# Kernel tuning notes

Measured on AMD Instinct MI355X. Metric: run time of the kernel, lower is better.

Reference implementation:

```python
import jax, jax.numpy as jnp
import numpy as np

N_NODES = 100000
N_EDGES = 1600000
N_ETYPES = 3
IN_FEATS = 128
HEADS = 4
OUT_FEATS = 16
EDGE_FEATS = 64
NEG_SLOPE = 0.2


def setup_inputs() -> dict:
    key = jax.random.key(0)
    ks = jax.random.split(key, 10)
    return {
        "x": jax.random.normal(ks[0], (N_NODES, IN_FEATS), jnp.float32),
        "W": jax.random.normal(ks[1], (IN_FEATS, HEADS * OUT_FEATS), jnp.float32) * 0.05,
        "W_e": jax.random.normal(ks[2], (EDGE_FEATS, HEADS * EDGE_FEATS), jnp.float32) * 0.05,
        "attn_l": jax.random.normal(ks[3], (HEADS, OUT_FEATS), jnp.float32) * 0.1,
        "attn_r": jax.random.normal(ks[4], (HEADS, OUT_FEATS), jnp.float32) * 0.1,
        "attn_e": jax.random.normal(ks[5], (HEADS, EDGE_FEATS), jnp.float32) * 0.1,
        "edge_emb": jax.random.normal(ks[6], (N_ETYPES, EDGE_FEATS), jnp.float32),
        "src": jax.random.randint(ks[7], (N_EDGES,), 0, N_NODES, jnp.int32),
        "dst": jax.random.randint(ks[8], (N_EDGES,), 0, N_NODES, jnp.int32),
        "etype": jax.random.randint(ks[9], (N_EDGES,), 0, N_ETYPES, jnp.int32),
    }


def reference(x, W, W_e, attn_l, attn_r, attn_e, edge_emb, src, dst, etype):
    N = x.shape[0]
    H, D = attn_l.shape
    # node projection: [N, H, D]
    feat = (x @ W).reshape(N, H, D)
    # per-node attention halves: [N, H]
    el = jnp.einsum("nhd,hd->nh", feat, attn_l)
    er = jnp.einsum("nhd,hd->nh", feat, attn_r)
    # per-etype edge term: [T, H]
    e_feat = (edge_emb @ W_e).reshape(edge_emb.shape[0], H, -1)
    ee = jnp.einsum("the,he->th", e_feat, attn_e)
    # per-edge pre-softmax score: [E, H]
    s = el[src] + er[dst] + ee[etype]
    s = jnp.where(s > 0, s, NEG_SLOPE * s)  # leaky_relu
    # edge softmax over incoming edges of each dst node (homogeneous graph)
    m = jax.ops.segment_max(s, dst, num_segments=N)
    e = jnp.exp(s - m[dst])
    z = jax.ops.segment_sum(e, dst, num_segments=N)
    a = e / z[dst]  # [E, H]
    # u_mul_e + sum aggregation: [N, H, D]
    msg = feat[src] * a[:, :, None]
    rst = jax.ops.segment_sum(msg, dst, num_segments=N)
    return rst, a
```

## Files before the change

kernel.cpp:

```cpp
#include <hip/hip_runtime.h>
#include <hip/hip_bf16.h>

#define N_NODES   100000
#define N_EDGES   1600000
#define N_ETYPES  3
#define IN_FEATS  128
#define HEADS     4
#define OUT_FEATS 16
#define EDGE_FEATS 64
#define HD        64
#define NEG_SLOPE 0.2f
#define MAXD_LDS  128

#define NBUCK     800
#define NPB       125
#define PBLK      400
#define EPB       4000
#define BCAP      2560


typedef short s16x8 __attribute__((ext_vector_type(8)));
typedef float f32x4 __attribute__((ext_vector_type(4)));

__device__ __forceinline__ short f2bs(float f) {
    __hip_bfloat16 h = __float2bfloat16(f);
    return *reinterpret_cast<short*>(&h);
}

__global__ __launch_bounds__(256) void wt_prep_kernel(
    const float* __restrict__ W, short* __restrict__ WTb)
{
    const int t = blockIdx.x * 256 + threadIdx.x;
    const int k = t >> 6, n = t & 63;
    WTb[n * IN_FEATS + k] = f2bs(W[t]);
}

#define XS_STRIDE 136
__global__ __launch_bounds__(256) void feat_el_er_kernel(
    const float* __restrict__ x,
    const short* __restrict__ WTb,
    const float* __restrict__ attn_l,
    const float* __restrict__ attn_r,
    __hip_bfloat16* __restrict__ featb,
    float* __restrict__ el,
    float* __restrict__ eriz)
{
    __shared__ short Xs[16 * XS_STRIDE];
    __shared__ short Ws[64 * XS_STRIDE];

    const int t = threadIdx.x;
    const int row0 = blockIdx.x * 16;
    {
        const int r = t >> 4, k0 = (t & 15) * 8;
        const float4* xg = (const float4*)(x + (size_t)(row0 + r) * IN_FEATS + k0);
        const float4 v0 = xg[0], v1 = xg[1];
        s16x8 p;
        p[0] = f2bs(v0.x); p[1] = f2bs(v0.y); p[2] = f2bs(v0.z); p[3] = f2bs(v0.w);
        p[4] = f2bs(v1.x); p[5] = f2bs(v1.y); p[6] = f2bs(v1.z); p[7] = f2bs(v1.w);
        *(s16x8*)&Xs[r * XS_STRIDE + k0] = p;
    }
    {
#pragma unroll
        for (int j = 0; j < 4; ++j) {
            const int u = t + 256 * j;
            const int r = u >> 4, c = (u & 15) * 8;
            *(s16x8*)&Ws[r * XS_STRIDE + c] = *(const s16x8*)(WTb + r * IN_FEATS + c);
        }
    }
    __syncthreads();

    const int w    = t >> 6;
    const int lane = t & 63;
    const int m    = lane & 15;
    const int q    = lane >> 4;

    f32x4 acc = {0.f, 0.f, 0.f, 0.f};
#pragma unroll
    for (int kb = 0; kb < 4; ++kb) {
        const s16x8 af = *(const s16x8*)&Xs[m * XS_STRIDE + kb * 32 + q * 8];
        const s16x8 bf = *(const s16x8*)&Ws[(w * 16 + m) * XS_STRIDE + kb * 32 + q * 8];
        acc = __builtin_amdgcn_mfma_f32_16x16x32_bf16(af, bf, acc, 0, 0, 0);
    }

    const float al = attn_l[w * OUT_FEATS + m];
    const float ar = attn_r[w * OUT_FEATS + m];
#pragma unroll
    for (int r = 0; r < 4; ++r) {
        const int row = row0 + q * 4 + r;
        featb[(size_t)row * HD + w * 16 + m] = __float2bfloat16(acc[r]);
        float cl = acc[r] * al;
        float cr = acc[r] * ar;
#pragma unroll
        for (int msk = 1; msk < 16; msk <<= 1) {
            cl += __shfl_xor(cl, msk, 64);
            cr += __shfl_xor(cr, msk, 64);
        }
        if (m == 0) {
            el[row * HEADS + w] = cl;
            eriz[(size_t)row * 8 + w] = cr;
        }
    }
}

__global__ __launch_bounds__(64) void ee_kernel(
    const float* __restrict__ edge_emb,
    const float* __restrict__ W_e,
    const float* __restrict__ attn_e,
    float* __restrict__ ee)
{
    const int b  = blockIdx.x;
    const int ty = b >> 2;
    const int h  = b & 3;
    const int e  = threadIdx.x;

    float ef = 0.f;
#pragma unroll
    for (int k = 0; k < EDGE_FEATS; ++k)
        ef += edge_emb[ty * EDGE_FEATS + k] *
              W_e[k * (HEADS * EDGE_FEATS) + h * EDGE_FEATS + e];
    float v = ef * attn_e[h * EDGE_FEATS + e];
#pragma unroll
    for (int m = 1; m < 64; m <<= 1) v += __shfl_xor(v, m, 64);
    if (e == 0) ee[ty * HEADS + h] = v;
}

__global__ __launch_bounds__(256) void bucket_hist_kernel(
    const int* __restrict__ dst, int* __restrict__ bhist)
{
    __shared__ int h[NBUCK];
    const int t = threadIdx.x, b = blockIdx.x;
    for (int j = t; j < NBUCK; j += 256) h[j] = 0;
    __syncthreads();
    const int e0 = b * EPB;
    for (int i = t; i < EPB; i += 256)
        atomicAdd(&h[dst[e0 + i] / NPB], 1);
    __syncthreads();
    for (int j = t; j < NBUCK; j += 256) bhist[b * NBUCK + j] = h[j];
}

__global__ __launch_bounds__(256) void bucket_scan1_kernel(
    int* __restrict__ bhist, int* __restrict__ btot)
{
    __shared__ int sh[PBLK];
    const int t = threadIdx.x, j = blockIdx.x;
    const int j0 = t, j1 = t + 256;
    int o0 = 0, o1 = 0;
    if (j0 < PBLK) { o0 = bhist[j0 * NBUCK + j]; sh[j0] = o0; }
    if (j1 < PBLK) { o1 = bhist[j1 * NBUCK + j]; sh[j1] = o1; }
    __syncthreads();
    for (int off = 1; off < PBLK; off <<= 1) {
        int v0 = (j0 >= off && j0 < PBLK) ? sh[j0 - off] : 0;
        int v1 = (j1 >= off && j1 < PBLK) ? sh[j1 - off] : 0;
        __syncthreads();
        if (j0 < PBLK) sh[j0] += v0;
        if (j1 < PBLK) sh[j1] += v1;
        __syncthreads();
    }
    if (j0 < PBLK) bhist[j0 * NBUCK + j] = sh[j0] - o0;
    if (j1 < PBLK) bhist[j1 * NBUCK + j] = sh[j1] - o1;
    if (t == 255) btot[j] = sh[PBLK - 1];
}

__global__ __launch_bounds__(1024) void bucket_scan2_kernel(
    const int* __restrict__ btot, int* __restrict__ bbase)
{
    __shared__ int sh[NBUCK];
    const int t = threadIdx.x;
    int o = 0;
    if (t < NBUCK) { o = btot[t]; sh[t] = o; }
    __syncthreads();
    for (int off = 1; off < NBUCK; off <<= 1) {
        int v = (t >= off && t < NBUCK) ? sh[t - off] : 0;
        __syncthreads();
        if (t < NBUCK) sh[t] += v;
        __syncthreads();
    }
    if (t < NBUCK) bbase[t] = sh[t] - o;
    if (t == NBUCK - 1) bbase[NBUCK] = sh[t];
}

__global__ __launch_bounds__(256) void bucket_scatter_kernel(
    const int* __restrict__ src, const int* __restrict__ dst,
    const int* __restrict__ etype,
    const int* __restrict__ bhist, const int* __restrict__ bbase,
    int* __restrict__ sc_bucket)
{
    __shared__ int cnt[NBUCK];
    const int t = threadIdx.x, b = blockIdx.x;
    for (int j = t; j < NBUCK; j += 256)
        cnt[j] = bbase[j] + bhist[b * NBUCK + j];
    __syncthreads();
    const int e0 = b * EPB;
    for (int i = t; i < EPB; i += 256) {
        const int e  = e0 + i;
        const int dn = dst[e];
        const int bu = dn / NPB;
        const int ld = dn - bu * NPB;
        const int slot = atomicAdd(&cnt[bu], 1);
        sc_bucket[slot] = src[e] | (etype[e] << 17) | (ld << 19);
    }
}

__global__ __launch_bounds__(256) void bucket_csr_kernel(
    const int* __restrict__ sc_bucket, const int* __restrict__ bbase,
    int* __restrict__ ptr, int* __restrict__ sc_csr)
{
    __shared__ int sbuf[BCAP];
    __shared__ int sdeg[128];
    __shared__ int scur[128];
    const int t = threadIdx.x, b = blockIdx.x;
    const int lo = bbase[b];
    const int count = bbase[b + 1] - lo;
    const bool staged = (count <= BCAP);

    if (t < 128) sdeg[t] = 0;
    __syncthreads();
    if (staged) {
        for (int i = t; i < count; i += 256) {
            const int v = sc_bucket[lo + i];
            sbuf[i] = v;
            atomicAdd(&sdeg[(v >> 19) & 0x7F], 1);
        }
    } else {
        for (int i = t; i < count; i += 256)
            atomicAdd(&sdeg[(sc_bucket[lo + i] >> 19) & 0x7F], 1);
    }
    __syncthreads();
    const int orig = (t < 128) ? sdeg[t] : 0;
    for (int off = 1; off < 128; off <<= 1) {
        const int v = (t < 128 && t >= off) ? sdeg[t - off] : 0;
        __syncthreads();
        if (t < 128) sdeg[t] += v;
        __syncthreads();
    }
    if (t < 128) {
        const int excl = sdeg[t] - orig;
        if (t < NPB) ptr[b * NPB + t] = lo + excl;
        scur[t] = lo + excl;
    }
    if (b == 0 && t == 0) ptr[N_NODES] = N_EDGES;
    __syncthreads();
    if (staged) {
        for (int i = t; i < count; i += 256) {
            const int v = sbuf[i];
            const int ld = (v >> 19) & 0x7F;
            const int slot = atomicAdd(&scur[ld], 1);
            sc_csr[slot] = v & 0x7FFFF;
        }
    } else {
        for (int i = t; i < count; i += 256) {
            const int v = sc_bucket[lo + i];
            const int ld = (v >> 19) & 0x7F;
            const int slot = atomicAdd(&scur[ld], 1);
            sc_csr[slot] = v & 0x7FFFF;
        }
    }
}

__global__ __launch_bounds__(256) void agg_kernel(
    const int* __restrict__ sc_csr, const int* __restrict__ ptr,
    const float* __restrict__ el, float* __restrict__ eriz,
    const float* __restrict__ ee, const __hip_bfloat16* __restrict__ featb,
    float* __restrict__ rst)
{
    __shared__ float w_lds[4][MAXD_LDS * HEADS];
    __shared__ int   s_lds[4][MAXD_LDS];
    const int wid  = threadIdx.x >> 6;
    const int lane = threadIdx.x & 63;
    const int n    = blockIdx.x * 4 + wid;

    const int p0  = ptr[n];
    const int deg = ptr[n + 1] - p0;
    float* wl = w_lds[wid];
    int*   sl = s_lds[wid];
    const ushort* fb = (const ushort*)featb;

    if (deg <= MAXD_LDS) {
        const int eo = lane >> 2;
        const int hA = lane & 3;
        const float er_n = eriz[(size_t)n * 8 + hA];
        const float g0 = ee[hA], g1 = ee[HEADS + hA], g2 = ee[2 * HEADS + hA];

        float zacc = 0.f;
        for (int i0 = 0; i0 < deg; i0 += 16) {
            const int idx = i0 + eo;
            if (idx < deg) {
                const int v  = sc_csr[p0 + idx];
                const int sn = v & 0x1FFFF;
                const int ty = v >> 17;
                float s = el[sn * HEADS + hA] + er_n +
                          ((ty == 0) ? g0 : ((ty == 1) ? g1 : g2));
                s = s > 0.f ? s : NEG_SLOPE * s;
                const float w = __expf(s);
                wl[idx * HEADS + hA] = w;
                if (hA == 0) sl[idx] = sn;
                zacc += w;
            }
        }
        zacc += __shfl_xor(zacc, 4, 64);
        zacc += __shfl_xor(zacc, 8, 64);
        zacc += __shfl_xor(zacc, 16, 64);
        zacc += __shfl_xor(zacc, 32, 64);
        if (lane < 4)
            eriz[(size_t)n * 8 + 4 + lane] = (deg > 0) ? __frcp_rn(zacc) : 0.f;

        const int q8 = lane >> 3;
        const int c8 = lane & 7;
        const int h8 = c8 >> 1;
        const float inv_z = (deg > 0) ? __frcp_rn(__shfl(zacc, h8, 64)) : 0.f;

        float a0 = 0.f, a1 = 0.f, a2 = 0.f, a3 = 0.f;
        float a4 = 0.f, a5 = 0.f, a6 = 0.f, a7 = 0.f;
        int i = 0;
        for (; i + 8 <= deg; i += 8) {
            const int idx = i + q8;
            const int sA = sl[idx];
            const float wA = wl[idx * HEADS + h8];
            const uint4 fA = *(const uint4*)(fb + ((size_t)sA << 6) + (c8 << 3));
            a0 += __uint_as_float(fA.x << 16) * wA;
            a1 += __uint_as_float(fA.x & 0xFFFF0000u) * wA;
            a2 += __uint_as_float(fA.y << 16) * wA;
            a3 += __uint_as_float(fA.y & 0xFFFF0000u) * wA;
            a4 += __uint_as_float(fA.z << 16) * wA;
            a5 += __uint_as_float(fA.z & 0xFFFF0000u) * wA;
            a6 += __uint_as_float(fA.w << 16) * wA;
            a7 += __uint_as_float(fA.w & 0xFFFF0000u) * wA;
        }
        if (i + q8 < deg) {
            const int idx = i + q8;
            const int sA = sl[idx];
            const float wA = wl[idx * HEADS + h8];
            const uint4 fA = *(const uint4*)(fb + ((size_t)sA << 6) + (c8 << 3));
            a0 += __uint_as_float(fA.x << 16) * wA;
            a1 += __uint_as_float(fA.x & 0xFFFF0000u) * wA;
            a2 += __uint_as_float(fA.y << 16) * wA;
            a3 += __uint_as_float(fA.y & 0xFFFF0000u) * wA;
            a4 += __uint_as_float(fA.z << 16) * wA;
            a5 += __uint_as_float(fA.z & 0xFFFF0000u) * wA;
            a6 += __uint_as_float(fA.w << 16) * wA;
            a7 += __uint_as_float(fA.w & 0xFFFF0000u) * wA;
        }
        a0 += __shfl_xor(a0, 8, 64); a0 += __shfl_xor(a0, 16, 64); a0 += __shfl_xor(a0, 32, 64);
        a1 += __shfl_xor(a1, 8, 64); a1 += __shfl_xor(a1, 16, 64); a1 += __shfl_xor(a1, 32, 64);
        a2 += __shfl_xor(a2, 8, 64); a2 += __shfl_xor(a2, 16, 64); a2 += __shfl_xor(a2, 32, 64);
        a3 += __shfl_xor(a3, 8, 64); a3 += __shfl_xor(a3, 16, 64); a3 += __shfl_xor(a3, 32, 64);
        a4 += __shfl_xor(a4, 8, 64); a4 += __shfl_xor(a4, 16, 64); a4 += __shfl_xor(a4, 32, 64);
        a5 += __shfl_xor(a5, 8, 64); a5 += __shfl_xor(a5, 16, 64); a5 += __shfl_xor(a5, 32, 64);
        a6 += __shfl_xor(a6, 8, 64); a6 += __shfl_xor(a6, 16, 64); a6 += __shfl_xor(a6, 32, 64);
        a7 += __shfl_xor(a7, 8, 64); a7 += __shfl_xor(a7, 16, 64); a7 += __shfl_xor(a7, 32, 64);
        if (q8 == 0) {
            f32x4 v0 = {a0 * inv_z, a1 * inv_z, a2 * inv_z, a3 * inv_z};
            f32x4 v1 = {a4 * inv_z, a5 * inv_z, a6 * inv_z, a7 * inv_z};
            *(f32x4*)(rst + (size_t)n * HD + (c8 << 3))     = v0;
            *(f32x4*)(rst + (size_t)n * HD + (c8 << 3) + 4) = v1;
        }
    } else {
        const int hA = lane & 3;
        const int eo = lane >> 2;
        const float er_nA = eriz[(size_t)n * 8 + hA];
        const float a0 = ee[hA], a1 = ee[HEADS + hA], a2 = ee[2 * HEADS + hA];
        float zacc = 0.f;
        for (int base = 0; base < deg; base += 16) {
            const int idx = base + eo;
            if (idx < deg) {
                const int v  = sc_csr[p0 + idx];
                const int sn = v & 0x1FFFF;
                const int ty = v >> 17;
                float s = el[sn * HEADS + hA] + er_nA + ((ty == 0) ? a0 : ((ty == 1) ? a1 : a2));
                s = s > 0.f ? s : NEG_SLOPE * s;
                zacc += __expf(s);
            }
        }
#pragma unroll
        for (int m = 4; m < 64; m <<= 1) zacc += __shfl_xor(zacc, m, 64);
        if (lane < 4) eriz[(size_t)n * 8 + 4 + lane] = __frcp_rn(zacc);
        const int h = lane >> 4;
        const float inv_z = __frcp_rn(__shfl(zacc, h, 64));
        const float er_n = eriz[(size_t)n * 8 + h];
        const float g0 = ee[h], g1 = ee[HEADS + h], g2 = ee[2 * HEADS + h];
        float racc = 0.f;
        for (int i = 0; i < deg; ++i) {
            const int v  = sc_csr[p0 + i];
            const int sn = v & 0x1FFFF;
            const int ty = v >> 17;
            float s = el[sn * HEADS + h] + er_n + ((ty == 0) ? g0 : ((ty == 1) ? g1 : g2));
            s = s > 0.f ? s : NEG_SLOPE * s;
            const float a = __expf(s) * inv_z;
            racc += __bfloat162float(featb[(size_t)sn * HD + lane]) * a;
        }
        rst[(size_t)n * HD + lane] = racc;
    }
}

__global__ __launch_bounds__(256) void attn_out_kernel(
    const int* __restrict__ src, const int* __restrict__ dst,
    const int* __restrict__ etype,
    const float* __restrict__ el, const float* __restrict__ eriz,
    const float* __restrict__ ee,
    float* __restrict__ a_out)
{
    const int e = blockIdx.x * 256 + threadIdx.x;
    const int sN = src[e];
    const int dN = dst[e];
    const int ty = etype[e];
    const float4 l4 = *(const float4*)(el + (size_t)sN * HEADS);
    const float4 r4 = *(const float4*)(eriz + (size_t)dN * 8);
    const float4 iz = *(const float4*)(eriz + (size_t)dN * 8 + 4);
    const float4 g4 = *(const float4*)(ee + (size_t)ty * HEADS);
    float4 a;
    float s;
    s = l4.x + r4.x + g4.x; s = s > 0.f ? s : NEG_SLOPE * s; a.x = __expf(s) * iz.x;
    s = l4.y + r4.y + g4.y; s = s > 0.f ? s : NEG_SLOPE * s; a.y = __expf(s) * iz.y;
    s = l4.z + r4.z + g4.z; s = s > 0.f ? s : NEG_SLOPE * s; a.z = __expf(s) * iz.z;
    s = l4.w + r4.w + g4.w; s = s > 0.f ? s : NEG_SLOPE * s; a.w = __expf(s) * iz.w;
    *(float4*)(a_out + (size_t)e * HEADS) = a;
}

extern "C" void kernel_launch(void* const* d_in, const int* in_sizes, int n_in,
                              void* d_out, int out_size, void* d_ws, size_t ws_size,
                              hipStream_t stream)
{
    const float* x        = (const float*)d_in[0];
    const float* W        = (const float*)d_in[1];
    const float* W_e      = (const float*)d_in[2];
    const float* attn_l   = (const float*)d_in[3];
    const float* attn_r   = (const float*)d_in[4];
    const float* attn_e   = (const float*)d_in[5];
    const float* edge_emb = (const float*)d_in[6];
    const int* src   = (const int*)d_in[7];
    const int* dst   = (const int*)d_in[8];
    const int* etype = (const int*)d_in[9];

    float* out     = (float*)d_out;
    float* rst_out = out;
    float* a_out   = out + (size_t)N_NODES * HD;

    char* w = (char*)d_ws;
    __hip_bfloat16* featb = (__hip_bfloat16*)w; w += (size_t)N_NODES * HD * 2;
    float* el    = (float*)w;  w += (size_t)N_NODES * HEADS * 4;
    float* eriz  = (float*)w;  w += (size_t)N_NODES * 8 * 4;
    float* ee    = (float*)w;  w += 64;
    int*   ptr   = (int*)w;    w += (size_t)(N_NODES + 4) * 4;
    int*   bhist = (int*)w;    w += (size_t)PBLK * NBUCK * 4;
    int*   btot  = (int*)w;    w += (size_t)NBUCK * 4;
    int*   bbase = (int*)w;    w += (size_t)(NBUCK + 4) * 4;
    short* WTb   = (short*)w;  w += (size_t)HD * IN_FEATS * 2;
    int*   sc_bucket = (int*)w; w += (size_t)N_EDGES * 4;
    int*   sc_csr    = (int*)w; w += (size_t)N_EDGES * 4;

    wt_prep_kernel<<<(IN_FEATS * HD) / 256, 256, 0, stream>>>(W, WTb);
    feat_el_er_kernel<<<N_NODES / 16, 256, 0, stream>>>(
        x, WTb, attn_l, attn_r, featb, el, eriz);
    ee_kernel<<<N_ETYPES * HEADS, 64, 0, stream>>>(edge_emb, W_e, attn_e, ee);

    bucket_hist_kernel<<<PBLK, 256, 0, stream>>>(dst, bhist);
    bucket_scan1_kernel<<<NBUCK, 256, 0, stream>>>(bhist, btot);
    bucket_scan2_kernel<<<1, 1024, 0, stream>>>(btot, bbase);
    bucket_scatter_kernel<<<PBLK, 256, 0, stream>>>(src, dst, etype, bhist, bbase, sc_bucket);
    bucket_csr_kernel<<<NBUCK, 256, 0, stream>>>(sc_bucket, bbase, ptr, sc_csr);

    agg_kernel<<<N_NODES / 4, 256, 0, stream>>>(
        sc_csr, ptr, el, eriz, ee, featb, rst_out);
    attn_out_kernel<<<N_EDGES / 256, 256, 0, stream>>>(
        src, dst, etype, el, eriz, ee, a_out);
}
```

Before: 287.9 us.

## Merge bucket-sort stages into one cooperative kernel and fold prep kernels

Replaces five separate bucket-sort kernel launches (histogram, two scans, scatter, CSR build) with a single cooperative kernel that separates the phases with grid-wide syncs. The per-edge-type ee computation becomes an extra block of the feature-projection kernel, and the W transpose/bf16 conversion now happens inside each projection block instead of in a separate prep kernel. The aim is to cut launch overhead and inter-kernel gaps, at the cost of grid-sync overhead, residency requirements for 800 cooperative blocks, and redundant strided W loads in every projection block.

After: 677.5 us. +135.3%, slower.

```diff
diff --git a/kernel.cpp b/kernel.cpp
--- a/kernel.cpp
+++ b/kernel.cpp
@@ -1,5 +1,8 @@
 #include <hip/hip_runtime.h>
 #include <hip/hip_bf16.h>
+#include <hip/hip_cooperative_groups.h>
+
+namespace cg = cooperative_groups;
 
 #define N_NODES   100000
 #define N_EDGES   1600000
@@ -27,28 +30,42 @@
     return *reinterpret_cast<short*>(&h);
 }
 
-__global__ __launch_bounds__(256) void wt_prep_kernel(
-    const float* __restrict__ W, short* __restrict__ WTb)
-{
-    const int t = blockIdx.x * 256 + threadIdx.x;
-    const int k = t >> 6, n = t & 63;
-    WTb[n * IN_FEATS + k] = f2bs(W[t]);
-}
-
 #define XS_STRIDE 136
 __global__ __launch_bounds__(256) void feat_el_er_kernel(
     const float* __restrict__ x,
-    const short* __restrict__ WTb,
+    const float* __restrict__ W,
     const float* __restrict__ attn_l,
     const float* __restrict__ attn_r,
+    const float* __restrict__ edge_emb,
+    const float* __restrict__ W_e,
+    const float* __restrict__ attn_e,
     __hip_bfloat16* __restrict__ featb,
     float* __restrict__ el,
-    float* __restrict__ eriz)
+    float* __restrict__ eriz,
+    float* __restrict__ ee)
 {
+    const int t = threadIdx.x;
+
+    if (blockIdx.x == N_NODES / 16) {
+        const int wv = t >> 6, e = t & 63;
+        for (int j = wv; j < N_ETYPES * HEADS; j += 4) {
+            const int ty = j >> 2, h = j & 3;
+            float ef = 0.f;
+#pragma unroll
+            for (int k = 0; k < EDGE_FEATS; ++k)
+                ef += edge_emb[ty * EDGE_FEATS + k] *
+                      W_e[k * (HEADS * EDGE_FEATS) + h * EDGE_FEATS + e];
+            float v = ef * attn_e[h * EDGE_FEATS + e];
+#pragma unroll
+            for (int m = 1; m < 64; m <<= 1) v += __shfl_xor(v, m, 64);
+            if (e == 0) ee[ty * HEADS + h] = v;
+        }
+        return;
+    }
+
     __shared__ short Xs[16 * XS_STRIDE];
     __shared__ short Ws[64 * XS_STRIDE];
 
-    const int t = threadIdx.x;
     const int row0 = blockIdx.x * 16;
     {
         const int r = t >> 4, k0 = (t & 15) * 8;
@@ -60,11 +77,15 @@
         *(s16x8*)&Xs[r * XS_STRIDE + k0] = p;
     }
     {
-#pragma unroll
-        for (int j = 0; j < 4; ++j) {
-            const int u = t + 256 * j;
-            const int r = u >> 4, c = (u & 15) * 8;
-            *(s16x8*)&Ws[r * XS_STRIDE + c] = *(const s16x8*)(WTb + r * IN_FEATS + c);
+        const int n  = t & 63;
+        const int kb = (t >> 6) * 32;
+#pragma unroll
+        for (int kk = 0; kk < 32; kk += 8) {
+            s16x8 p;
+#pragma unroll
+            for (int j = 0; j < 8; ++j)
+                p[j] = f2bs(W[(size_t)(kb + kk + j) * HD + n]);
+            *(s16x8*)&Ws[n * XS_STRIDE + kb + kk] = p;
         }
     }
     __syncthreads();
@@ -102,157 +123,143 @@
     }
 }
 
-__global__ __launch_bounds__(64) void ee_kernel(
-    const float* __restrict__ edge_emb,
-    const float* __restrict__ W_e,
-    const float* __restrict__ attn_e,
-    float* __restrict__ ee)
-{
-    const int b  = blockIdx.x;
-    const int ty = b >> 2;
-    const int h  = b & 3;
-    const int e  = threadIdx.x;
-
-    float ef = 0.f;
-#pragma unroll
-    for (int k = 0; k < EDGE_FEATS; ++k)
-        ef += edge_emb[ty * EDGE_FEATS + k] *
-              W_e[k * (HEADS * EDGE_FEATS) + h * EDGE_FEATS + e];
-    float v = ef * attn_e[h * EDGE_FEATS + e];
-#pragma unroll
-    for (int m = 1; m < 64; m <<= 1) v += __shfl_xor(v, m, 64);
-    if (e == 0) ee[ty * HEADS + h] = v;
-}
-
-__global__ __launch_bounds__(256) void bucket_hist_kernel(
-    const int* __restrict__ dst, int* __restrict__ bhist)
-{
-    __shared__ int h[NBUCK];
-    const int t = threadIdx.x, b = blockIdx.x;
-    for (int j = t; j < NBUCK; j += 256) h[j] = 0;
-    __syncthreads();
-    const int e0 = b * EPB;
-    for (int i = t; i < EPB; i += 256)
-        atomicAdd(&h[dst[e0 + i] / NPB], 1);
-    __syncthreads();
-    for (int j = t; j < NBUCK; j += 256) bhist[b * NBUCK + j] = h[j];
-}
-
-__global__ __launch_bounds__(256) void bucket_scan1_kernel(
-    int* __restrict__ bhist, int* __restrict__ btot)
-{
-    __shared__ int sh[PBLK];
-    const int t = threadIdx.x, j = blockIdx.x;
-    const int j0 = t, j1 = t + 256;
-    int o0 = 0, o1 = 0;
-    if (j0 < PBLK) { o0 = bhist[j0 * NBUCK + j]; sh[j0] = o0; }
-    if (j1 < PBLK) { o1 = bhist[j1 * NBUCK + j]; sh[j1] = o1; }
-    __syncthreads();
-    for (int off = 1; off < PBLK; off <<= 1) {
-        int v0 = (j0 >= off && j0 < PBLK) ? sh[j0 - off] : 0;
-        int v1 = (j1 >= off && j1 < PBLK) ? sh[j1 - off] : 0;
-        __syncthreads();
-        if (j0 < PBLK) sh[j0] += v0;
-        if (j1 < PBLK) sh[j1] += v1;
-        __syncthreads();
-    }
-    if (j0 < PBLK) bhist[j0 * NBUCK + j] = sh[j0] - o0;
-    if (j1 < PBLK) bhist[j1 * NBUCK + j] = sh[j1] - o1;
-    if (t == 255) btot[j] = sh[PBLK - 1];
-}
-
-__global__ __launch_bounds__(1024) void bucket_scan2_kernel(
-    const int* __restrict__ btot, int* __restrict__ bbase)
-{
-    __shared__ int sh[NBUCK];
-    const int t = threadIdx.x;
-    int o = 0;
-    if (t < NBUCK) { o = btot[t]; sh[t] = o; }
-    __syncthreads();
-    for (int off = 1; off < NBUCK; off <<= 1) {
-        int v = (t >= off && t < NBUCK) ? sh[t - off] : 0;
-        __syncthreads();
-        if (t < NBUCK) sh[t] += v;
-        __syncthreads();
-    }
-    if (t < NBUCK) bbase[t] = sh[t] - o;
-    if (t == NBUCK - 1) bbase[NBUCK] = sh[t];
-}
-
-__global__ __launch_bounds__(256) void bucket_scatter_kernel(
+__global__ __launch_bounds__(256, 4) void coop_sort_kernel(
     const int* __restrict__ src, const int* __restrict__ dst,
     const int* __restrict__ etype,
-    const int* __restrict__ bhist, const int* __restrict__ bbase,
-    int* __restrict__ sc_bucket)
+    int* __restrict__ bhist, int* __restrict__ btot, int* __restrict__ bbase,
+    int* __restrict__ ptr, int* __restrict__ sc_bucket, int* __restrict__ sc_csr)
 {
-    __shared__ int cnt[NBUCK];
+    cg::grid_group grid = cg::this_grid();
+    __shared__ int smem[BCAP + 256];
     const int t = threadIdx.x, b = blockIdx.x;
-    for (int j = t; j < NBUCK; j += 256)
-        cnt[j] = bbase[j] + bhist[b * NBUCK + j];
-    __syncthreads();
-    const int e0 = b * EPB;
-    for (int i = t; i < EPB; i += 256) {
-        const int e  = e0 + i;
-        const int dn = dst[e];
-        const int bu = dn / NPB;
-        const int ld = dn - bu * NPB;
-        const int slot = atomicAdd(&cnt[bu], 1);
-        sc_bucket[slot] = src[e] | (etype[e] << 17) | (ld << 19);
-    }
-}
-
-__global__ __launch_bounds__(256) void bucket_csr_kernel(
-    const int* __restrict__ sc_bucket, const int* __restrict__ bbase,
-    int* __restrict__ ptr, int* __restrict__ sc_csr)
-{
-    __shared__ int sbuf[BCAP];
-    __shared__ int sdeg[128];
-    __shared__ int scur[128];
-    const int t = threadIdx.x, b = blockIdx.x;
-    const int lo = bbase[b];
-    const int count = bbase[b + 1] - lo;
-    const bool staged = (count <= BCAP);
-
-    if (t < 128) sdeg[t] = 0;
-    __syncthreads();
-    if (staged) {
-        for (int i = t; i < count; i += 256) {
-            const int v = sc_bucket[lo + i];
-            sbuf[i] = v;
-            atomicAdd(&sdeg[(v >> 19) & 0x7F], 1);
-        }
-    } else {
-        for (int i = t; i < count; i += 256)
-            atomicAdd(&sdeg[(sc_bucket[lo + i] >> 19) & 0x7F], 1);
-    }
-    __syncthreads();
-    const int orig = (t < 128) ? sdeg[t] : 0;
-    for (int off = 1; off < 128; off <<= 1) {
-        const int v = (t < 128 && t >= off) ? sdeg[t - off] : 0;
-        __syncthreads();
-        if (t < 128) sdeg[t] += v;
-        __syncthreads();
-    }
-    if (t < 128) {
-        const int excl = sdeg[t] - orig;
-        if (t < NPB) ptr[b * NPB + t] = lo + excl;
-        scur[t] = lo + excl;
-    }
-    if (b == 0 && t == 0) ptr[N_NODES] = N_EDGES;
-    __syncthreads();
-    if (staged) {
-        for (int i = t; i < count; i += 256) {
-            const int v = sbuf[i];
-            const int ld = (v >> 19) & 0x7F;
-            const int slot = atomicAdd(&scur[ld], 1);
-            sc_csr[slot] = v & 0x7FFFF;
-        }
-    } else {
-        for (int i = t; i < count; i += 256) {
-            const int v = sc_bucket[lo + i];
-            const int ld = (v >> 19) & 0x7F;
-            const int slot = atomicAdd(&scur[ld], 1);
-            sc_csr[slot] = v & 0x7FFFF;
+
+    if (b < PBLK) {
+        int* h = smem;
+        for (int j = t; j < NBUCK; j += 256) h[j] = 0;
+        __syncthreads();
+        const int e0 = b * EPB;
+        for (int i = t; i < EPB; i += 256)
+            atomicAdd(&h[dst[e0 + i] / NPB], 1);
+        __syncthreads();
+        for (int j = t; j < NBUCK; j += 256) bhist[b * NBUCK + j] = h[j];
+    }
+    grid.sync();
+
+    {
+        int* sh = smem;
+        const int j = b;
+        const int j0 = t, j1 = t + 256;
+        int o0 = 0, o1 = 0;
+        if (j0 < PBLK) { o0 = bhist[j0 * NBUCK + j]; sh[j0] = o0; }
+        if (j1 < PBLK) { o1 = bhist[j1 * NBUCK + j]; sh[j1] = o1; }
+        __syncthreads();
+        for (int off = 1; off < PBLK; off <<= 1) {
+            int v0 = (j0 >= off && j0 < PBLK) ? sh[j0 - off] : 0;
+            int v1 = (j1 >= off && j1 < PBLK) ? sh[j1 - off] : 0;
+            __syncthreads();
+            if (j0 < PBLK) sh[j0] += v0;
+            if (j1 < PBLK) sh[j1] += v1;
+            __syncthreads();
+        }
+        if (j0 < PBLK) bhist[j0 * NBUCK + j] = sh[j0] - o0;
+        if (j1 < PBLK) bhist[j1 * NBUCK + j] = sh[j1] - o1;
+        if (t == 255) btot[j] = sh[PBLK - 1];
+    }
+    grid.sync();
+
+    if (b == 0) {
+        int e0 = 0, e1 = 0, e2 = 0, e3 = 0;
+        if (t < NBUCK / 4) {
+            e0 = btot[4 * t];     e1 = btot[4 * t + 1];
+            e2 = btot[4 * t + 2]; e3 = btot[4 * t + 3];
+        }
+        const int tsum = e0 + e1 + e2 + e3;
+        int* sh = smem;
+        sh[t] = tsum;
+        __syncthreads();
+        for (int off = 1; off < 256; off <<= 1) {
+            const int v = (t >= off) ? sh[t - off] : 0;
+            __syncthreads();
+            sh[t] += v;
+            __syncthreads();
+        }
+        const int excl = sh[t] - tsum;
+        if (t < NBUCK / 4) {
+            bbase[4 * t]     = excl;
+            bbase[4 * t + 1] = excl + e0;
+            bbase[4 * t + 2] = excl + e0 + e1;
+            bbase[4 * t + 3] = excl + e0 + e1 + e2;
+        }
+        if (t == 255) bbase[NBUCK] = sh[255];
+    }
+    grid.sync();
+
+    if (b < PBLK) {
+        int* cnt = smem;
+        for (int j = t; j < NBUCK; j += 256)
+            cnt[j] = bbase[j] + bhist[b * NBUCK + j];
+        __syncthreads();
+        const int e0 = b * EPB;
+        for (int i = t; i < EPB; i += 256) {
+            const int e  = e0 + i;
+            const int dn = dst[e];
+            const int bu = dn / NPB;
+            const int ld = dn - bu * NPB;
+            const int slot = atomicAdd(&cnt[bu], 1);
+            sc_bucket[slot] = src[e] | (etype[e] << 17) | (ld << 19);
+        }
+    }
+    grid.sync();
+
+    {
+        int* sbuf = smem;
+        int* sdeg = smem + BCAP;
+        int* scur = smem + BCAP + 128;
+        const int lo = bbase[b];
+        const int count = bbase[b + 1] - lo;
+        const bool staged = (count <= BCAP);
+
+        if (t < 128) sdeg[t] = 0;
+        __syncthreads();
+        if (staged) {
+            for (int i = t; i < count; i += 256) {
+                const int v = sc_bucket[lo + i];
+                sbuf[i] = v;
+                atomicAdd(&sdeg[(v >> 19) & 0x7F], 1);
+            }
+        } else {
+            for (int i = t; i < count; i += 256)
+                atomicAdd(&sdeg[(sc_bucket[lo + i] >> 19) & 0x7F], 1);
+        }
+        __syncthreads();
+        const int orig = (t < 128) ? sdeg[t] : 0;
+        for (int off = 1; off < 128; off <<= 1) {
+            const int v = (t < 128 && t >= off) ? sdeg[t - off] : 0;
+            __syncthreads();
+            if (t < 128) sdeg[t] += v;
+            __syncthreads();
+        }
+        if (t < 128) {
+            const int excl = sdeg[t] - orig;
+            if (t < NPB) ptr[b * NPB + t] = lo + excl;
+            scur[t] = lo + excl;
+        }
+        if (b == 0 && t == 0) ptr[N_NODES] = N_EDGES;
+        __syncthreads();
+        if (staged) {
+            for (int i = t; i < count; i += 256) {
+                const int v = sbuf[i];
+                const int ld = (v >> 19) & 0x7F;
+                const int slot = atomicAdd(&scur[ld], 1);
+                sc_csr[slot] = v & 0x7FFFF;
+            }
+        } else {
+            for (int i = t; i < count; i += 256) {
+                const int v = sc_bucket[lo + i];
+                const int ld = (v >> 19) & 0x7F;
+                const int slot = atomicAdd(&scur[ld], 1);
+                sc_csr[slot] = v & 0x7FFFF;
+            }
         }
     }
 }
@@ -444,23 +451,25 @@
     int*   bhist = (int*)w;    w += (size_t)PBLK * NBUCK * 4;
     int*   btot  = (int*)w;    w += (size_t)NBUCK * 4;
     int*   bbase = (int*)w;    w += (size_t)(NBUCK + 4) * 4;
-    short* WTb   = (short*)w;  w += (size_t)HD * IN_FEATS * 2;
     int*   sc_bucket = (int*)w; w += (size_t)N_EDGES * 4;
     int*   sc_csr    = (int*)w; w += (size_t)N_EDGES * 4;
 
-    wt_prep_kernel<<<(IN_FEATS * HD) / 256, 256, 0, stream>>>(W, WTb);
-    feat_el_er_kernel<<<N_NODES / 16, 256, 0, stream>>>(
-        x, WTb, attn_l, attn_r, featb, el, eriz);
-    ee_kernel<<<N_ETYPES * HEADS, 64, 0, stream>>>(edge_emb, W_e, attn_e, ee);
-
-    bucket_hist_kernel<<<PBLK, 256, 0, stream>>>(dst, bhist);
-    bucket_scan1_kernel<<<NBUCK, 256, 0, stream>>>(bhist, btot);
-    bucket_scan2_kernel<<<1, 1024, 0, stream>>>(btot, bbase);
-    bucket_scatter_kernel<<<PBLK, 256, 0, stream>>>(src, dst, etype, bhist, bbase, sc_bucket);
-    bucket_csr_kernel<<<NBUCK, 256, 0, stream>>>(sc_bucket, bbase, ptr, sc_csr);
+    feat_el_er_kernel<<<N_NODES / 16 + 1, 256, 0, stream>>>(
+        x, W, attn_l, attn_r, edge_emb, W_e, attn_e, featb, el, eriz, ee);
+
+    {
+        void* cargs[] = {
+            (void*)&src, (void*)&dst, (void*)&etype,
+            (void*)&bhist, (void*)&btot, (void*)&bbase,
+            (void*)&ptr, (void*)&sc_bucket, (void*)&sc_csr
+        };
+        hipLaunchCooperativeKernel((const void*)coop_sort_kernel,
+                                   dim3(NBUCK), dim3(256), cargs, 0, stream);
+    }
 
     agg_kernel<<<N_NODES / 4, 256, 0, stream>>>(
         sc_csr, ptr, el, eriz, ee, featb, rst_out);
+
     attn_out_kernel<<<N_EDGES / 256, 256, 0, stream>>>(
         src, dst, etype, el, eriz, ee, a_out);
 }
```
